# Kernel tuning notes

Measured on AMD Instinct MI355X. Metric: run time of the kernel, lower is better.

Reference implementation:

```python
import jax, jax.numpy as jnp
import numpy as np

KH = KW = 3
K = KH * KW
MAX_S, MIN_S = 3.0, 0.5
A_S = (MAX_S - MIN_S) / 2.0   # 1.25
B_S = (MAX_S + MIN_S) / 2.0   # 1.75


def _conv3x3(x, w, b):
    # x: [B,C,H,W], w: [O,C,3,3], b: [O]
    y = jax.lax.conv_general_dilated(
        x, w, window_strides=(1, 1), padding='SAME',
        dimension_numbers=('NCHW', 'OIHW', 'NCHW'))
    return y + b[None, :, None, None]


def setup_inputs() -> dict:
    key = jax.random.key(0)
    ks = jax.random.split(key, 6)
    b, c_in, c_out, h, w = 2, 64, 64, 192, 192
    x = jax.random.normal(ks[0], (b, c_in, h, w), jnp.float32)
    w_main = jax.random.normal(ks[1], (c_out, c_in, KH, KW), jnp.float32) * 0.05
    # offset-branch params (randomized, small, so offsets are non-trivial)
    w_rot = jax.random.normal(ks[2], (2, c_in, 3, 3), jnp.float32) * 0.05
    b_rot = jnp.array([0.0, 1.0], jnp.float32)  # init_angle=0 -> (sin,cos)=(0,1)
    w_str = jax.random.normal(ks[3], (1, c_in, 3, 3), jnp.float32) * 0.05
    b_str = jnp.zeros((1,), jnp.float32)
    w_whole = jax.random.normal(ks[4], (1, c_in, 3, 3), jnp.float32) * 0.05
    b_whole = jnp.zeros((1,), jnp.float32)
    return dict(x=x, w_main=w_main, w_rot=w_rot, b_rot=b_rot,
                w_str=w_str, b_str=b_str, w_whole=w_whole, b_whole=b_whole)


def reference(x, w_main, w_rot, b_rot, w_str, b_str, w_whole, b_whole):
    bsz, cin, H, W = x.shape
    # base kernel offsets (row-major over 3x3, centered): di rows, dj cols
    di = jnp.array([-1, -1, -1, 0, 0, 0, 1, 1, 1], jnp.float32)  # [K]
    dj = jnp.array([-1, 0, 1, -1, 0, 1, -1, 0, 1], jnp.float32)  # [K]

    # per-pixel rotation (normalized sin/cos)
    rot = _conv3x3(x, w_rot, b_rot)          # [B,2,H,W]
    sin, cos = rot[:, 0], rot[:, 1]          # [B,H,W]
    norm = jnp.sqrt(sin * sin + cos * cos + 1e-6)
    sin, cos = sin / norm, cos / norm

    # stretch on the row coordinate, bounded by tanh into [MIN_S, MAX_S]
    r = jnp.tanh(_conv3x3(x, w_str, b_str))[:, 0] * A_S + B_S   # [B,H,W]
    # whole-grid rescale >= 1
    wr = 1.0 + jax.nn.relu(_conv3x3(x, w_whole, b_whole))[:, 0]  # [B,H,W]

    # banded offsets before rotation: row comp scaled by r*wr, col by wr
    bd0 = di * (r * wr)[..., None]           # [B,H,W,K]
    bd1 = dj * wr[..., None]                 # [B,H,W,K]
    # rotation matrix [[cos, sin], [-sin, cos]] @ [bd0; bd1], minus base
    off_y = cos[..., None] * bd0 + sin[..., None] * bd1 - di     # [B,H,W,K]
    off_x = -sin[..., None] * bd0 + cos[..., None] * bd1 - dj    # [B,H,W,K]

    # sampling positions: p = out_pos - pad + tap + offset; (tap - pad) == di/dj
    py = jnp.arange(H, dtype=jnp.float32)[None, :, None, None] + di + off_y
    px = jnp.arange(W, dtype=jnp.float32)[None, None, :, None] + dj + off_x

    # bilinear gather with zero padding outside the image
    x_bhwc = x.transpose(0, 2, 3, 1)         # [B,H,W,C]
    y0 = jnp.floor(py)
    x0 = jnp.floor(px)
    ty = py - y0
    tx = px - x0
    y0i = y0.astype(jnp.int32)
    x0i = x0.astype(jnp.int32)
    bidx = jnp.arange(bsz)[:, None, None, None]

    def gather(yi, xi):
        valid = ((yi >= 0) & (yi < H) & (xi >= 0) & (xi < W)).astype(x.dtype)
        v = x_bhwc[bidx, jnp.clip(yi, 0, H - 1), jnp.clip(xi, 0, W - 1)]  # [B,H,W,K,C]
        return v * valid[..., None]

    sampled = (gather(y0i, x0i) * ((1 - ty) * (1 - tx))[..., None]
               + gather(y0i, x0i + 1) * ((1 - ty) * tx)[..., None]
               + gather(y0i + 1, x0i) * (ty * (1 - tx))[..., None]
               + gather(y0i + 1, x0i + 1) * (ty * tx)[..., None])  # [B,H,W,K,C]

    w_flat = w_main.reshape(w_main.shape[0], w_main.shape[1], K)   # [O,C,K]
    out = jnp.einsum('bhwkc,ock->bohw', sampled, w_flat)
    return out
```

## Files before the change

### kernel.cpp

```cpp
#include <hip/hip_runtime.h>
#include <hip/hip_bf16.h>
#include <stdint.h>

typedef unsigned short u16;
typedef unsigned int   u32;

#define HH 192
#define WW 192
#define HWSZ (192*192)
#define NPIX (2*HWSZ)

typedef __attribute__((ext_vector_type(8))) short short8;
typedef __attribute__((ext_vector_type(4))) float floatx4;

__device__ __forceinline__ float bflo(u32 u){ union{u32 i; float f;} v; v.i = u<<16; return v.f; }
__device__ __forceinline__ float bfhi(u32 u){ union{u32 i; float f;} v; v.i = u & 0xffff0000u; return v.f; }
__device__ __forceinline__ float bf2f(u16 u){ union{u32 i; float f;} v; v.i = ((u32)u)<<16; return v.f; }
__device__ __forceinline__ u16 f2bf(float f){
    union{float f; u32 i;} v; v.f = f;
    u32 b = v.i;
    u32 r = b + 0x7fffu + ((b>>16)&1u);
    return (u16)(r>>16);
}

__device__ __forceinline__ int sniff_fp32(const void* x) {
    const u32* x32 = (const u32*)x;
    int l = threadIdx.x & 63;
    u32 v = x32[l*2];
    u32 e = (v >> 7) & 0xFFu;
    int vote = (e >= 0x60u && e <= 0x8Fu) ? 1 : 0;
    unsigned long long m = __ballot(vote);
    return (__popcll(m) < 40) ? 1 : 0;
}

__device__ __forceinline__ u16 pick16(const void* p, int i, int fp32) {
    return fp32 ? f2bf(((const float*)p)[i]) : ((const u16*)p)[i];
}
__device__ __forceinline__ float pickf(const void* p, int i, int fp32) {
    return fp32 ? ((const float*)p)[i] : bf2f(((const u16*)p)[i]);
}

__global__ __launch_bounds__(256) void k0_prep(const void* __restrict__ x,
                        const void* __restrict__ wm,
                        const void* __restrict__ wrot,
                        const void* __restrict__ brot,
                        const void* __restrict__ wstr,
                        const void* __restrict__ bstr,
                        const void* __restrict__ wwh,
                        const void* __restrict__ bwh,
                        u16* __restrict__ bfrag, float* __restrict__ wf) {
    int fp32 = sniff_fp32(x);
    int e = blockIdx.x*256 + threadIdx.x;
    if (e < 9*2*4*64*8) {
        int j    = e & 7;
        int lane = (e>>3) & 63;
        int wd   = (e>>9) & 3;
        int kk   = (e>>11) & 1;
        int k    = e>>12;
        int o = wd*16 + (lane & 15);
        int c = kk*32 + ((lane>>4)&3)*8 + j;
        bfrag[e] = pick16(wm, (o*64 + c)*9 + k, fp32);
    }
    if (e < 9216) {
        int j   = e & 3;
        int rem = e >> 2;
        int tap = rem % 9;
        int c   = rem / 9;
        float s;
        if (j==0)      s = pickf(wrot, c*9 + tap, fp32);
        else if (j==1) s = pickf(wrot, (64+c)*9 + tap, fp32);
        else if (j==2) s = pickf(wstr, c*9 + tap, fp32);
        else           s = pickf(wwh,  c*9 + tap, fp32);
        wf[e] = s;
    }
    if (e < 4) {
        float bv;
        if (e==0)      bv = pickf(brot, 0, fp32);
        else if (e==1) bv = pickf(brot, 1, fp32);
        else if (e==2) bv = pickf(bstr, 0, fp32);
        else           bv = pickf(bwh,  0, fp32);
        wf[9216 + e] = bv;
    }
}

__global__ __launch_bounds__(256) void k1_transpose(const void* __restrict__ x, u16* __restrict__ xt) {
    int fp32 = sniff_fp32(x);
    int gp = blockIdx.x*256 + threadIdx.x;
    int b = gp / HWSZ, hw = gp % HWSZ;
    u32 vr[32];
    if (fp32) {
        const float* src = (const float*)x + (size_t)b*64*HWSZ + hw;
#pragma unroll
        for (int i = 0; i < 32; i++) {
            u32 lo = f2bf(src[(size_t)(2*i)*HWSZ]);
            u32 hi = f2bf(src[(size_t)(2*i+1)*HWSZ]);
            vr[i] = lo | (hi<<16);
        }
    } else {
        const u16* src = (const u16*)x + (size_t)b*64*HWSZ + hw;
#pragma unroll
        for (int i = 0; i < 32; i++) {
            u32 lo = src[(size_t)(2*i)*HWSZ];
            u32 hi = src[(size_t)(2*i+1)*HWSZ];
            vr[i] = lo | (hi<<16);
        }
    }
    uint4* dst = (uint4*)(xt + (size_t)gp*64);
#pragma unroll
    for (int i = 0; i < 8; i++)
        dst[i] = make_uint4(vr[4*i], vr[4*i+1], vr[4*i+2], vr[4*i+3]);
}

__global__ __launch_bounds__(256) void k2_fields(const void* __restrict__ x, const float* __restrict__ wf,
                          float4* __restrict__ fields) {
    __shared__ float4 red[256];
    int fp32 = sniff_fp32(x);
    int t = threadIdx.x;
    int q = t >> 6, p = t & 63;
    int gp0 = blockIdx.x * 64;
    int gp = gp0 + p;
    int b = gp / HWSZ, hw = gp % HWSZ;
    int h = hw / WW, w = hw % WW;
    float a0=0.f, a1=0.f, a2=0.f, a3=0.f;
    const float4* wf4 = (const float4*)wf;
    if (fp32) {
        const float* xf = (const float*)x;
#pragma unroll 1
        for (int c16 = 0; c16 < 16; c16++) {
            int c = q*16 + c16;
            size_t plane = (size_t)(b*64 + c)*HWSZ;
#pragma unroll
            for (int kh = 0; kh < 3; kh++) {
                int y = h + kh - 1;
                if ((unsigned)y >= (unsigned)HH) continue;
#pragma unroll
                for (int kw = 0; kw < 3; kw++) {
                    int xx = w + kw - 1;
                    if ((unsigned)xx >= (unsigned)WW) continue;
                    float v = xf[plane + (size_t)y*WW + xx];
                    float4 wv = wf4[c*9 + kh*3 + kw];
                    a0 = fmaf(v, wv.x, a0);
                    a1 = fmaf(v, wv.y, a1);
                    a2 = fmaf(v, wv.z, a2);
                    a3 = fmaf(v, wv.w, a3);
                }
            }
        }
    } else {
        const u16* xu = (const u16*)x;
#pragma unroll 1
        for (int c16 = 0; c16 < 16; c16++) {
            int c = q*16 + c16;
            size_t plane = (size_t)(b*64 + c)*HWSZ;
#pragma unroll
            for (int kh = 0; kh < 3; kh++) {
                int y = h + kh - 1;
                if ((unsigned)y >= (unsigned)HH) continue;
#pragma unroll
                for (int kw = 0; kw < 3; kw++) {
                    int xx = w + kw - 1;
                    if ((unsigned)xx >= (unsigned)WW) continue;
                    float v = bf2f(xu[plane + (size_t)y*WW + xx]);
                    float4 wv = wf4[c*9 + kh*3 + kw];
                    a0 = fmaf(v, wv.x, a0);
                    a1 = fmaf(v, wv.y, a1);
                    a2 = fmaf(v, wv.z, a2);
                    a3 = fmaf(v, wv.w, a3);
                }
            }
        }
    }
    red[t] = make_float4(a0, a1, a2, a3);
    __syncthreads();
    if (t < 64) {
        float4 r0 = red[t], r1 = red[t+64], r2 = red[t+128], r3 = red[t+192];
        float s0 = r0.x + r1.x + r2.x + r3.x;
        float s1 = r0.y + r1.y + r2.y + r3.y;
        float s2 = r0.z + r1.z + r2.z + r3.z;
        float s3 = r0.w + r1.w + r2.w + r3.w;
        float sr = s0 + wf[9216];
        float cr = s1 + wf[9217];
        float inv = 1.0f / sqrtf(sr*sr + cr*cr + 1e-6f);
        float r  = tanhf(s2 + wf[9218])*1.25f + 1.75f;
        float wrv = 1.0f + fmaxf(s3 + wf[9219], 0.0f);
        fields[gp0 + t] = make_float4(sr*inv, cr*inv, r*wrv, wrv);
    }
}

__device__ __forceinline__ void load16(const u16* base, u32 r[8]) {
    const uint4* p = (const uint4*)base;
    uint4 a = p[0], b = p[1];
    r[0]=a.x; r[1]=a.y; r[2]=a.z; r[3]=a.w;
    r[4]=b.x; r[5]=b.y; r[6]=b.z; r[7]=b.w;
}

__global__ __launch_bounds__(256) void k3_main(const void* __restrict__ xorig,
                                               const u16* __restrict__ xt,
                                               const float4* __restrict__ fields,
                                               const u16* __restrict__ bfrag,
                                               void* __restrict__ out) {
    __shared__ u16 samp[64*72];

    int fp32 = sniff_fp32(xorig);
    int t = threadIdx.x;
    int pix0 = blockIdx.x * 64;
    int b   = pix0 / HWSZ;
    int hw0 = pix0 % HWSZ;

    int p = t >> 2, q = t & 3;
    int hw = hw0 + p;
    int h = hw / WW, w = hw % WW;
    float4 f = fields[pix0 + p];
    float sn = f.x, cs = f.y, rwr = f.z, wr = f.w;
    const u16* xbase = xt + (size_t)b*HWSZ*64;

    int wd = t >> 6, lane = t & 63;
    int quad = lane >> 4, l15 = lane & 15;
    floatx4 acc[4];
#pragma unroll
    for (int i=0;i<4;i++) acc[i] = (floatx4){0.f,0.f,0.f,0.f};
    const short8* bfr = (const short8*)bfrag;

#pragma unroll 1
    for (int k = 0; k < 9; k++) {
        int di = k/3 - 1;
        int dj = k - (k/3)*3 - 1;
        float bd0 = (float)di * rwr;
        float bd1 = (float)dj * wr;
        float py = (float)h + cs*bd0 + sn*bd1;
        float px = (float)w - sn*bd0 + cs*bd1;
        float y0f = floorf(py), x0f = floorf(px);
        float ty = py - y0f, tx = px - x0f;
        int y0 = (int)y0f, x0 = (int)x0f;
        int y1 = y0 + 1,   x1 = x0 + 1;
        float fy0 = (y0>=0 && y0<HH) ? 1.f : 0.f;
        float fy1 = (y1>=0 && y1<HH) ? 1.f : 0.f;
        float fx0 = (x0>=0 && x0<WW) ? 1.f : 0.f;
        float fx1 = (x1>=0 && x1<WW) ? 1.f : 0.f;
        int yc0 = min(max(y0,0),HH-1), yc1 = min(max(y1,0),HH-1);
        int xc0 = min(max(x0,0),WW-1), xc1 = min(max(x1,0),WW-1);
        float w00 = (1.f-ty)*(1.f-tx)*fy0*fx0;
        float w01 = (1.f-ty)*tx      *fy0*fx1;
        float w10 = ty      *(1.f-tx)*fy1*fx0;
        float w11 = ty      *tx      *fy1*fx1;

        u32 r00[8], r01[8], r10[8], r11[8];
        const u16* row0 = xbase + (size_t)(yc0*WW)*64 + q*16;
        const u16* row1 = xbase + (size_t)(yc1*WW)*64 + q*16;
        load16(row0 + xc0*64, r00);
        load16(row0 + xc1*64, r01);
        load16(row1 + xc0*64, r10);
        load16(row1 + xc1*64, r11);

        u32 packed[8];
#pragma unroll
        for (int d=0; d<8; d++) {
            float s0 = w00*bflo(r00[d]) + w01*bflo(r01[d]) + w10*bflo(r10[d]) + w11*bflo(r11[d]);
            float s1 = w00*bfhi(r00[d]) + w01*bfhi(r01[d]) + w10*bfhi(r10[d]) + w11*bfhi(r11[d]);
            packed[d] = ((u32)f2bf(s0)) | (((u32)f2bf(s1))<<16);
        }
        uint4* dst = (uint4*)&samp[p*72 + q*16];
        dst[0] = make_uint4(packed[0],packed[1],packed[2],packed[3]);
        dst[1] = make_uint4(packed[4],packed[5],packed[6],packed[7]);
        __syncthreads();

        short8 b0 = bfr[((k*2+0)*4 + wd)*64 + lane];
        short8 b1 = bfr[((k*2+1)*4 + wd)*64 + lane];
#pragma unroll
        for (int mt=0; mt<4; mt++) {
            int pr = mt*16 + l15;
            short8 a0 = *(const short8*)&samp[pr*72 +      quad*8];
            short8 a1 = *(const short8*)&samp[pr*72 + 32 + quad*8];
            acc[mt] = __builtin_amdgcn_mfma_f32_16x16x32_bf16(a0, b0, acc[mt], 0, 0, 0);
            acc[mt] = __builtin_amdgcn_mfma_f32_16x16x32_bf16(a1, b1, acc[mt], 0, 0, 0);
        }
        __syncthreads();
    }

    {
        int o = wd*16 + l15;
#pragma unroll
        for (int mt=0; mt<4; mt++)
#pragma unroll
            for (int rg=0; rg<4; rg++) {
                int pxi = mt*16 + quad*4 + rg;
                samp[o*72 + pxi] = f2bf(acc[mt][rg]);
            }
    }
    __syncthreads();
    {
        int o = t >> 2, q2 = t & 3;
        const uint4* s = (const uint4*)&samp[o*72 + q2*16];
        uint4 v0 = s[0], v1 = s[1];
        size_t base = (size_t)(b*64 + o)*HWSZ + hw0 + q2*16;
        if (fp32) {
            float4* df = (float4*)((float*)out + base);
            df[0] = make_float4(bflo(v0.x), bfhi(v0.x), bflo(v0.y), bfhi(v0.y));
            df[1] = make_float4(bflo(v0.z), bfhi(v0.z), bflo(v0.w), bfhi(v0.w));
            df[2] = make_float4(bflo(v1.x), bfhi(v1.x), bflo(v1.y), bfhi(v1.y));
            df[3] = make_float4(bflo(v1.z), bfhi(v1.z), bflo(v1.w), bfhi(v1.w));
        } else {
            uint4* du = (uint4*)((u16*)out + base);
            du[0] = v0; du[1] = v1;
        }
    }
}

extern "C" void kernel_launch(void* const* d_in, const int* in_sizes, int n_in,
                              void* d_out, int out_size, void* d_ws, size_t ws_size,
                              hipStream_t stream) {
    const void* x    = d_in[0];
    const void* wm   = d_in[1];
    const void* wrot = d_in[2];
    const void* brot = d_in[3];
    const void* wstr = d_in[4];
    const void* bstr = d_in[5];
    const void* wwh  = d_in[6];
    const void* bwh  = d_in[7];

    char* ws = (char*)d_ws;
    u16*    xt     = (u16*)   (ws);
    float4* fields = (float4*)(ws + 9437184);
    u16*    bfrag  = (u16*)   (ws + 10616832);
    float*  wf     = (float*) (ws + 10690560);

    k0_prep     <<<dim3(144),  dim3(256), 0, stream>>>(x, wm, wrot, brot, wstr, bstr, wwh, bwh, bfrag, wf);
    k1_transpose<<<dim3(288),  dim3(256), 0, stream>>>(x, xt);
    k2_fields   <<<dim3(1152), dim3(256), 0, stream>>>(x, wf, fields);
    k3_main     <<<dim3(1152), dim3(256), 0, stream>>>(x, xt, (const float4*)fields, bfrag, d_out);
}
```

Before: 175.7 us.

## Double-buffer sampled tile in main kernel, vectorize transpose, branchless field conv

The main kernel now double-buffers the shared sample tile, so the gather and bilinear blend for the next tap overlap the MFMAs on the current one, with one barrier per tap instead of two. The transpose kernel handles two pixels per thread with float2/u32 loads and half the blocks. The fields conv precomputes clamped offsets and masks so the loop has no branches and can be partially unrolled. bf16 packing uses the hardware conversion intrinsic. The cost is higher register and LDS use per block, which may lower occupancy.

Result: slower. 186.1 us (+5.9%).

```diff
diff --git a/kernel.cpp b/kernel.cpp
--- a/kernel.cpp
+++ b/kernel.cpp
@@ -21,6 +21,10 @@
     u32 b = v.i;
     u32 r = b + 0x7fffu + ((b>>16)&1u);
     return (u16)(r>>16);
+}
+__device__ __forceinline__ u32 pkbf(float a, float b){
+    __hip_bfloat162 h = __float22bfloat162_rn(make_float2(a, b));
+    union { __hip_bfloat162 h; u32 u; } cv; cv.h = h; return cv.u;
 }
 
 __device__ __forceinline__ int sniff_fp32(const void* x) {
@@ -85,30 +89,36 @@
 
 __global__ __launch_bounds__(256) void k1_transpose(const void* __restrict__ x, u16* __restrict__ xt) {
     int fp32 = sniff_fp32(x);
-    int gp = blockIdx.x*256 + threadIdx.x;
+    int s = blockIdx.x*256 + threadIdx.x;
+    int gp = s*2;
     int b = gp / HWSZ, hw = gp % HWSZ;
-    u32 vr[32];
+    u32 v0[32], v1[32];
     if (fp32) {
         const float* src = (const float*)x + (size_t)b*64*HWSZ + hw;
 #pragma unroll
         for (int i = 0; i < 32; i++) {
-            u32 lo = f2bf(src[(size_t)(2*i)*HWSZ]);
-            u32 hi = f2bf(src[(size_t)(2*i+1)*HWSZ]);
-            vr[i] = lo | (hi<<16);
+            float2 la = *(const float2*)(src + (size_t)(2*i)*HWSZ);
+            float2 lb = *(const float2*)(src + (size_t)(2*i+1)*HWSZ);
+            v0[i] = pkbf(la.x, lb.x);
+            v1[i] = pkbf(la.y, lb.y);
         }
     } else {
-        const u16* src = (const u16*)x + (size_t)b*64*HWSZ + hw;
+        const u16* srcu = (const u16*)x + (size_t)b*64*HWSZ + hw;
 #pragma unroll
         for (int i = 0; i < 32; i++) {
-            u32 lo = src[(size_t)(2*i)*HWSZ];
-            u32 hi = src[(size_t)(2*i+1)*HWSZ];
-            vr[i] = lo | (hi<<16);
-        }
-    }
-    uint4* dst = (uint4*)(xt + (size_t)gp*64);
-#pragma unroll
-    for (int i = 0; i < 8; i++)
-        dst[i] = make_uint4(vr[4*i], vr[4*i+1], vr[4*i+2], vr[4*i+3]);
+            u32 la = *(const u32*)(srcu + (size_t)(2*i)*HWSZ);
+            u32 lb = *(const u32*)(srcu + (size_t)(2*i+1)*HWSZ);
+            v0[i] = (la & 0xFFFFu) | (lb << 16);
+            v1[i] = (la >> 16)     | (lb & 0xFFFF0000u);
+        }
+    }
+    uint4* d0 = (uint4*)(xt + (size_t)gp*64);
+    uint4* d1 = (uint4*)(xt + (size_t)(gp+1)*64);
+#pragma unroll
+    for (int i = 0; i < 8; i++) {
+        d0[i] = make_uint4(v0[4*i], v0[4*i+1], v0[4*i+2], v0[4*i+3]);
+        d1[i] = make_uint4(v1[4*i], v1[4*i+1], v1[4*i+2], v1[4*i+3]);
+    }
 }
 
 __global__ __launch_bounds__(256) void k2_fields(const void* __restrict__ x, const float* __restrict__ wf,
@@ -121,52 +131,53 @@
     int gp = gp0 + p;
     int b = gp / HWSZ, hw = gp % HWSZ;
     int h = hw / WW, w = hw % WW;
+
+    int   off[9];
+    float msk[9];
+#pragma unroll
+    for (int kh = 0; kh < 3; kh++) {
+        int y   = h + kh - 1;
+        int yok = ((unsigned)y < (unsigned)HH) ? 1 : 0;
+        int yc  = min(max(y,0),HH-1);
+#pragma unroll
+        for (int kw = 0; kw < 3; kw++) {
+            int xx  = w + kw - 1;
+            int xok = ((unsigned)xx < (unsigned)WW) ? 1 : 0;
+            off[kh*3+kw] = yc*WW + min(max(xx,0),WW-1);
+            msk[kh*3+kw] = (yok & xok) ? 1.0f : 0.0f;
+        }
+    }
+
     float a0=0.f, a1=0.f, a2=0.f, a3=0.f;
-    const float4* wf4 = (const float4*)wf;
+    const float4* wrow = (const float4*)wf + (size_t)q*16*9;
     if (fp32) {
-        const float* xf = (const float*)x;
-#pragma unroll 1
+        const float* xp = (const float*)x + (size_t)(b*64 + q*16)*HWSZ;
+#pragma unroll 4
         for (int c16 = 0; c16 < 16; c16++) {
-            int c = q*16 + c16;
-            size_t plane = (size_t)(b*64 + c)*HWSZ;
-#pragma unroll
-            for (int kh = 0; kh < 3; kh++) {
-                int y = h + kh - 1;
-                if ((unsigned)y >= (unsigned)HH) continue;
-#pragma unroll
-                for (int kw = 0; kw < 3; kw++) {
-                    int xx = w + kw - 1;
-                    if ((unsigned)xx >= (unsigned)WW) continue;
-                    float v = xf[plane + (size_t)y*WW + xx];
-                    float4 wv = wf4[c*9 + kh*3 + kw];
-                    a0 = fmaf(v, wv.x, a0);
-                    a1 = fmaf(v, wv.y, a1);
-                    a2 = fmaf(v, wv.z, a2);
-                    a3 = fmaf(v, wv.w, a3);
-                }
+            const float* pl = xp + (size_t)c16*HWSZ;
+#pragma unroll
+            for (int i = 0; i < 9; i++) {
+                float v = pl[off[i]] * msk[i];
+                float4 wv = wrow[c16*9 + i];
+                a0 = fmaf(v, wv.x, a0);
+                a1 = fmaf(v, wv.y, a1);
+                a2 = fmaf(v, wv.z, a2);
+                a3 = fmaf(v, wv.w, a3);
             }
         }
     } else {
-        const u16* xu = (const u16*)x;
-#pragma unroll 1
+        const u16* xp = (const u16*)x + (size_t)(b*64 + q*16)*HWSZ;
+#pragma unroll 4
         for (int c16 = 0; c16 < 16; c16++) {
-            int c = q*16 + c16;
-            size_t plane = (size_t)(b*64 + c)*HWSZ;
-#pragma unroll
-            for (int kh = 0; kh < 3; kh++) {
-                int y = h + kh - 1;
-                if ((unsigned)y >= (unsigned)HH) continue;
-#pragma unroll
-                for (int kw = 0; kw < 3; kw++) {
-                    int xx = w + kw - 1;
-                    if ((unsigned)xx >= (unsigned)WW) continue;
-                    float v = bf2f(xu[plane + (size_t)y*WW + xx]);
-                    float4 wv = wf4[c*9 + kh*3 + kw];
-                    a0 = fmaf(v, wv.x, a0);
-                    a1 = fmaf(v, wv.y, a1);
-                    a2 = fmaf(v, wv.z, a2);
-                    a3 = fmaf(v, wv.w, a3);
-                }
+            const u16* pl = xp + (size_t)c16*HWSZ;
+#pragma unroll
+            for (int i = 0; i < 9; i++) {
+                float v = bf2f(pl[off[i]]) * msk[i];
+                float4 wv = wrow[c16*9 + i];
+                a0 = fmaf(v, wv.x, a0);
+                a1 = fmaf(v, wv.y, a1);
+                a2 = fmaf(v, wv.z, a2);
+                a3 = fmaf(v, wv.w, a3);
             }
         }
     }
@@ -199,7 +210,7 @@
                                                const float4* __restrict__ fields,
                                                const u16* __restrict__ bfrag,
                                                void* __restrict__ out) {
-    __shared__ u16 samp[64*72];
+    __shared__ u16 samp[2][64*72];
 
     int fp32 = sniff_fp32(xorig);
     int t = threadIdx.x;
@@ -221,10 +232,12 @@
     for (int i=0;i<4;i++) acc[i] = (floatx4){0.f,0.f,0.f,0.f};
     const short8* bfr = (const short8*)bfrag;
 
-#pragma unroll 1
-    for (int k = 0; k < 9; k++) {
+    u32 r00[8], r01[8], r10[8], r11[8];
+    float w00, w01, w10, w11;
+
+    auto coords_load = [&](int k) {
         int di = k/3 - 1;
-        int dj = k - (k/3)*3 - 1;
+        int dj = k%3 - 1;
         float bd0 = (float)di * rwr;
         float bd1 = (float)dj * wr;
         float py = (float)h + cs*bd0 + sn*bd1;
@@ -233,49 +246,58 @@
         float ty = py - y0f, tx = px - x0f;
         int y0 = (int)y0f, x0 = (int)x0f;
         int y1 = y0 + 1,   x1 = x0 + 1;
-        float fy0 = (y0>=0 && y0<HH) ? 1.f : 0.f;
-        float fy1 = (y1>=0 && y1<HH) ? 1.f : 0.f;
-        float fx0 = (x0>=0 && x0<WW) ? 1.f : 0.f;
-        float fx1 = (x1>=0 && x1<WW) ? 1.f : 0.f;
+        float fy0 = ((unsigned)y0 < (unsigned)HH) ? 1.f : 0.f;
+        float fy1 = ((unsigned)y1 < (unsigned)HH) ? 1.f : 0.f;
+        float fx0 = ((unsigned)x0 < (unsigned)WW) ? 1.f : 0.f;
+        float fx1 = ((unsigned)x1 < (unsigned)WW) ? 1.f : 0.f;
         int yc0 = min(max(y0,0),HH-1), yc1 = min(max(y1,0),HH-1);
         int xc0 = min(max(x0,0),WW-1), xc1 = min(max(x1,0),WW-1);
-        float w00 = (1.f-ty)*(1.f-tx)*fy0*fx0;
-        float w01 = (1.f-ty)*tx      *fy0*fx1;
-        float w10 = ty      *(1.f-tx)*fy1*fx0;
-        float w11 = ty      *tx      *fy1*fx1;
-
-        u32 r00[8], r01[8], r10[8], r11[8];
+        w00 = (1.f-ty)*(1.f-tx)*fy0*fx0;
+        w01 = (1.f-ty)*tx      *fy0*fx1;
+        w10 = ty      *(1.f-tx)*fy1*fx0;
+        w11 = ty      *tx      *fy1*fx1;
         const u16* row0 = xbase + (size_t)(yc0*WW)*64 + q*16;
         const u16* row1 = xbase + (size_t)(yc1*WW)*64 + q*16;
         load16(row0 + xc0*64, r00);
         load16(row0 + xc1*64, r01);
         load16(row1 + xc0*64, r10);
         load16(row1 + xc1*64, r11);
-
+    };
+
+    auto blend_store = [&](int buf) {
         u32 packed[8];
 #pragma unroll
         for (int d=0; d<8; d++) {
             float s0 = w00*bflo(r00[d]) + w01*bflo(r01[d]) + w10*bflo(r10[d]) + w11*bflo(r11[d]);
             float s1 = w00*bfhi(r00[d]) + w01*bfhi(r01[d]) + w10*bfhi(r10[d]) + w11*bfhi(r11[d]);
-            packed[d] = ((u32)f2bf(s0)) | (((u32)f2bf(s1))<<16);
-        }
-        uint4* dst = (uint4*)&samp[p*72 + q*16];
+            packed[d] = pkbf(s0, s1);
+        }
+        uint4* dst = (uint4*)&samp[buf][p*72 + q*16];
         dst[0] = make_uint4(packed[0],packed[1],packed[2],packed[3]);
         dst[1] = make_uint4(packed[4],packed[5],packed[6],packed[7]);
+    };
+
+    coords_load(0);
+    blend_store(0);
+
+#pragma unroll 1
+    for (int k = 0; k < 9; k++) {
         __syncthreads();
-
+        if (k < 8) coords_load(k+1);
         short8 b0 = bfr[((k*2+0)*4 + wd)*64 + lane];
         short8 b1 = bfr[((k*2+1)*4 + wd)*64 + lane];
+        const u16* sb = samp[k & 1];
 #pragma unroll
         for (int mt=0; mt<4; mt++) {
             int pr = mt*16 + l15;
-            short8 a0 = *(const short8*)&samp[pr*72 +      quad*8];
-            short8 a1 = *(const short8*)&samp[pr*72 + 32 + quad*8];
+            short8 a0 = *(const short8*)&sb[pr*72 +      quad*8];
+            short8 a1 = *(const short8*)&sb[pr*72 + 32 + quad*8];
             acc[mt] = __builtin_amdgcn_mfma_f32_16x16x32_bf16(a0, b0, acc[mt], 0, 0, 0);
             acc[mt] = __builtin_amdgcn_mfma_f32_16x16x32_bf16(a1, b1, acc[mt], 0, 0, 0);
         }
-        __syncthreads();
-    }
+        if (k < 8) blend_store((k+1) & 1);
+    }
+    __syncthreads();
 
     {
         int o = wd*16 + l15;
@@ -284,13 +306,13 @@
 #pragma unroll
             for (int rg=0; rg<4; rg++) {
                 int pxi = mt*16 + quad*4 + rg;
-                samp[o*72 + pxi] = f2bf(acc[mt][rg]);
+                samp[0][o*72 + pxi] = f2bf(acc[mt][rg]);
             }
     }
     __syncthreads();
     {
         int o = t >> 2, q2 = t & 3;
-        const uint4* s = (const uint4*)&samp[o*72 + q2*16];
+        const uint4* s = (const uint4*)&samp[0][o*72 + q2*16];
         uint4 v0 = s[0], v1 = s[1];
         size_t base = (size_t)(b*64 + o)*HWSZ + hw0 + q2*16;
         if (fp32) {
@@ -325,7 +347,7 @@
     float*  wf     = (float*) (ws + 10690560);
 
     k0_prep     <<<dim3(144),  dim3(256), 0, stream>>>(x, wm, wrot, brot, wstr, bstr, wwh, bwh, bfrag, wf);
-    k1_transpose<<<dim3(288),  dim3(256), 0, stream>>>(x, xt);
+    k1_transpose<<<dim3(144),  dim3(256), 0, stream>>>(x, xt);
     k2_fields   <<<dim3(1152), dim3(256), 0, stream>>>(x, wf, fields);
     k3_main     <<<dim3(1152), dim3(256), 0, stream>>>(x, xt, (const float4*)fields, bfrag, d_out);
 }
```
